# Performance work log

Measured on AMD Instinct MI355X. Metric: run time of the kernel, lower is better.

## Reference

```python
import jax, jax.numpy as jnp
import numpy as np

EPS = 1e-12

def _normalize(v):
    # matches F.normalize(..., eps): v / max(||v||, eps)
    return v / jnp.maximum(jnp.linalg.norm(v), EPS)

def sn_weight(W, u):
    """One power iteration (num_svs=1, num_itrs=1, eval mode: u not updated).
    W: [out, in] (1x1 conv flattened). u: [1, out].
    u, v are no-grad in torch; sv = v @ W.T @ u'.T carries grad w.r.t. W."""
    v = jax.lax.stop_gradient(_normalize(jax.lax.stop_gradient(u) @ W))          # [1, in]
    u2 = jax.lax.stop_gradient(_normalize(v @ W.T))                              # [1, out]
    sv = (v @ W.T @ u2.T)[0, 0]
    return W / sv

def maxpool2x2(x):
    B, C, H, W = x.shape
    return x.reshape(B, C, H // 2, 2, W // 2, 2).max(axis=(3, 5))

def conv1x1(W, x):
    # W: [out_c, in_c], x: [B, in_c, H, W]
    return jnp.einsum('oc,bchw->bohw', W, x)

def setup_inputs() -> dict:
    key = jax.random.key(0)
    ks = jax.random.split(key, 9)
    ch = 128
    B, H, W = 16, 64, 64
    x = jax.random.normal(ks[0], (B, ch, H, W), dtype=jnp.float32)
    # 1x1 conv weights flattened to [out, in], kaiming-ish scale
    def w(k, o, i):
        return jax.random.normal(k, (o, i), dtype=jnp.float32) * (1.0 / np.sqrt(i))
    w_theta = w(ks[1], ch // 8, ch)
    w_phi   = w(ks[2], ch // 8, ch)
    w_g     = w(ks[3], ch // 2, ch)
    w_o     = w(ks[4], ch, ch // 2)
    u_theta = jax.random.normal(ks[5], (1, ch // 8), dtype=jnp.float32)
    u_phi   = jax.random.normal(ks[6], (1, ch // 8), dtype=jnp.float32)
    u_g     = jax.random.normal(ks[7], (1, ch // 2), dtype=jnp.float32)
    u_o     = jax.random.normal(ks[8], (1, ch), dtype=jnp.float32)
    gamma = jnp.float32(0.7)  # param (init 0.0 in torch; nonzero for a meaningful test)
    return dict(x=x, w_theta=w_theta, w_phi=w_phi, w_g=w_g, w_o=w_o,
                u_theta=u_theta, u_phi=u_phi, u_g=u_g, u_o=u_o, gamma=gamma)

def reference(x, w_theta, w_phi, w_g, w_o, u_theta, u_phi, u_g, u_o, gamma):
    B, C, H, W = x.shape
    Wt = sn_weight(w_theta, u_theta)
    Wp = sn_weight(w_phi, u_phi)
    Wg = sn_weight(w_g, u_g)
    Wo = sn_weight(w_o, u_o)
    theta = conv1x1(Wt, x).reshape(B, C // 8, H * W)               # [B, C/8, HW]
    phi = maxpool2x2(conv1x1(Wp, x)).reshape(B, C // 8, H * W // 4)  # [B, C/8, HW/4]
    g = maxpool2x2(conv1x1(Wg, x)).reshape(B, C // 2, H * W // 4)    # [B, C/2, HW/4]
    beta = jax.nn.softmax(jnp.einsum('bcs,bct->bst', theta, phi), axis=-1)  # [B, HW, HW/4]
    o = jnp.einsum('bct,bst->bcs', g, beta).reshape(B, C // 2, H, W)
    return gamma * conv1x1(Wo, o) + x
```

## Files before the change

### kernel.cpp

```cpp
#include <hip/hip_runtime.h>
#include <hip/hip_bf16.h>


#define U_WN  0
#define U_WO  12288
#define U_TH  20480
#define U_PHI 1069056
#define U_G   1331200

typedef __attribute__((ext_vector_type(8))) short bf16x8;
typedef __attribute__((ext_vector_type(4))) short s16x4;
typedef __attribute__((ext_vector_type(4))) float f32x4;
typedef __attribute__((ext_vector_type(16))) float f32x16;

__device__ inline unsigned short f2b(float f) {
    union { float f; unsigned u; } v; v.f = f;
    unsigned r = v.u + 0x7FFFu + ((v.u >> 16) & 1u);
    return (unsigned short)(r >> 16);
}
__device__ inline float b2f(unsigned short u) {
    union { unsigned u; float f; } v; v.u = ((unsigned)u) << 16; return v.f;
}

__device__ inline unsigned cvtpk_bf16(float lo, float hi) {
    unsigned r;
    asm("s_nop 0\n\tv_cvt_pk_bf16_f32 %0, %1, %2" : "=v"(r) : "v"(lo), "v"(hi));
    return r;
}
__device__ inline void pl32swap(unsigned &a, unsigned &b) {
    asm("s_nop 1\n\tv_permlane32_swap_b32 %0, %1\n\ts_nop 1" : "+v"(a), "+v"(b));
}

__global__ __launch_bounds__(256) void sn4(
        const float* __restrict__ w0, const float* __restrict__ w1,
        const float* __restrict__ w2, const float* __restrict__ w3,
        const float* __restrict__ u0, const float* __restrict__ u1,
        const float* __restrict__ u2, const float* __restrict__ u3,
        unsigned short* __restrict__ wsu) {
    int wi = blockIdx.x;
    const float* W; const float* u; unsigned short* dst; int on, in_;
    if      (wi == 0) { W = w0; u = u0; dst = wsu;          on = 16;  in_ = 128; }
    else if (wi == 1) { W = w1; u = u1; dst = wsu + 2048;   on = 16;  in_ = 128; }
    else if (wi == 2) { W = w2; u = u2; dst = wsu + 4096;   on = 64;  in_ = 128; }
    else              { W = w3; u = u3; dst = wsu + 12288;  on = 128; in_ = 64;  }
    __shared__ float Wl[8320];
    __shared__ float ul[128];
    __shared__ float v[128];
    __shared__ float red[256];
    __shared__ float s_inv;
    int tid = threadIdx.x;
    int n = on * in_;
    int stride = in_ + 1;
    int shift = (in_ == 128) ? 7 : 6;
    int mask = in_ - 1;
    for (int i = tid; i < n; i += 256) {
        int o = i >> shift, j = i & mask;
        Wl[o * stride + j] = W[i];
    }
    if (tid < on) ul[tid] = u[tid];
    __syncthreads();
    float vi = 0.f;
    if (tid < in_) {
        for (int o = 0; o < on; ++o) vi += ul[o] * Wl[o * stride + tid];
    }
    red[tid] = (tid < in_) ? vi * vi : 0.f;
    __syncthreads();
    for (int st = 128; st > 0; st >>= 1) {
        if (tid < st) red[tid] += red[tid + st];
        __syncthreads();
    }
    float inv_nv = 1.0f / fmaxf(sqrtf(red[0]), 1e-12f);
    __syncthreads();
    if (tid < in_) v[tid] = vi * inv_nv;
    __syncthreads();
    float ui = 0.f;
    if (tid < on) {
        for (int i = 0; i < in_; ++i) ui += v[i] * Wl[tid * stride + i];
    }
    red[tid] = (tid < on) ? ui * ui : 0.f;
    __syncthreads();
    for (int st = 128; st > 0; st >>= 1) {
        if (tid < st) red[tid] += red[tid + st];
        __syncthreads();
    }
    if (tid == 0) {
        float nsq = red[0];
        float sv = nsq / fmaxf(sqrtf(nsq), 1e-12f);
        s_inv = 1.0f / sv;
    }
    __syncthreads();
    float inv = s_inv;
    for (int e = tid; e < n; e += 256) {
        int o = e >> shift, j = e & mask;
        dst[e] = f2b(Wl[o * stride + j] * inv);
    }
}

__global__ __launch_bounds__(512, 4) void convpool_mfma(
        const float* __restrict__ x, const unsigned short* __restrict__ wn,
        unsigned short* __restrict__ thetaT, unsigned short* __restrict__ phiT,
        unsigned short* __restrict__ gT) {
    __shared__ unsigned short xT[128 * 136];
    __shared__ unsigned short wnl[96 * 136];
    int tid = threadIdx.x;
    int bb = blockIdx.x >> 5, tile = blockIdx.x & 31;
    int px0 = tile << 7;
    for (int i = tid; i < 1536; i += 512) {
        int r = i >> 4, c8 = (i & 15) * 8;
        *(bf16x8*)&wnl[r * 136 + c8] = *(const bf16x8*)&wn[r * 128 + c8];
    }
    const float4* x4 = (const float4*)x;
    {
        int p4 = tid & 31, cg = (tid >> 5) * 4;
        for (int k = 0; k < 2; ++k) {
            int cb = k * 64 + cg;
            float4 v0 = x4[(bb * 128 + cb + 0) * 1024 + tile * 32 + p4];
            float4 v1 = x4[(bb * 128 + cb + 1) * 1024 + tile * 32 + p4];
            float4 v2 = x4[(bb * 128 + cb + 2) * 1024 + tile * 32 + p4];
            float4 v3 = x4[(bb * 128 + cb + 3) * 1024 + tile * 32 + p4];
            float a0[4] = {v0.x, v0.y, v0.z, v0.w};
            float a1[4] = {v1.x, v1.y, v1.z, v1.w};
            float a2[4] = {v2.x, v2.y, v2.z, v2.w};
            float a3[4] = {v3.x, v3.y, v3.z, v3.w};
#pragma unroll
            for (int j = 0; j < 4; ++j) {
                union { unsigned w[2]; s16x4 v; } pk;
                pk.w[0] = cvtpk_bf16(a0[j], a1[j]);
                pk.w[1] = cvtpk_bf16(a2[j], a3[j]);
                *(s16x4*)&xT[(p4 * 4 + j) * 136 + cb] = pk.v;
            }
        }
    }
    __syncthreads();
    int lane = tid & 63, wv = tid >> 6;
    int q = lane >> 4, l = lane & 15;
    int pxw = wv * 16;
    f32x4 acc[6];
    const f32x4 z4 = {0.f, 0.f, 0.f, 0.f};
#pragma unroll
    for (int nt = 0; nt < 6; ++nt) acc[nt] = z4;
#pragma unroll
    for (int kk = 0; kk < 4; ++kk) {
        bf16x8 a0 = *(const bf16x8*)&xT[(pxw + l) * 136 + kk * 32 + q * 8];
#pragma unroll
        for (int nt = 0; nt < 6; ++nt) {
            bf16x8 bw = *(const bf16x8*)&wnl[(nt * 16 + l) * 136 + kk * 32 + q * 8];
            acc[nt] = __builtin_amdgcn_mfma_f32_16x16x32_bf16(a0, bw, acc[nt], 0, 0, 0);
        }
    }
#pragma unroll
    for (int r = 0; r < 4; ++r) {
        int s = px0 + pxw + q * 4 + r;
        thetaT[(bb * 4096 + s) * 16 + l] = f2b(acc[0][r]);
    }
    __syncthreads();
    unsigned short* poolbuf = wnl;
#pragma unroll
    for (int nt = 1; nt < 6; ++nt) {
        int ch = nt * 16 + l - 16;
#pragma unroll
        for (int r = 0; r < 4; ++r) {
            poolbuf[ch * 132 + pxw + q * 4 + r] = f2b(acc[nt][r]);
        }
    }
    __syncthreads();
    for (int i = tid; i < 2560; i += 512) {
        int tcol = i & 31, ch = i >> 5;
        int base = ch * 132 + tcol * 2;
        float m0 = fmaxf(b2f(poolbuf[base]), b2f(poolbuf[base + 1]));
        float m1 = fmaxf(b2f(poolbuf[base + 64]), b2f(poolbuf[base + 65]));
        float m = fmaxf(m0, m1);
        int t = tile * 32 + tcol;
        if (ch < 16) phiT[(bb * 1024 + t) * 16 + ch] = f2b(m);
        else         gT[(bb * 64 + ch - 16) * 1024 + t] = f2b(m);
    }
}

__global__ __launch_bounds__(256, 4) void attn_out(
        const unsigned short* __restrict__ thetaT,
        const unsigned short* __restrict__ phiT,
        const unsigned short* __restrict__ gT,
        const unsigned short* __restrict__ wo,
        const float* __restrict__ x, const float* __restrict__ gam,
        float* __restrict__ out) {
    __shared__ unsigned short gl[2][2][4096];
    __shared__ float ldsD[2][2][32];
    float* ldsOf = (float*)&gl[0][0][0];
    int tid = threadIdx.x;
    int kblk = blockIdx.x;
    int vblk = (kblk & 7) * 128 + (kblk >> 3);
    int bb = vblk >> 6, st = vblk & 63;
    int s0 = st << 6;
    int lane = tid & 63, wv = tid >> 6;
    int sg = wv & 1, sp = wv >> 1;
    int sl = lane & 31, hi = lane >> 5;
    int srow = bb * 4096 + s0 + sg * 32 + sl;
    const unsigned short* phiB = phiT + bb * 16384;
    const unsigned short* gB   = gT + bb * 65536;
    int tbase = sp << 9;

    int sidx = tid & 127, shalf = tid >> 7;
    int src_c = sidx >> 1, spos = sidx & 1;
    const unsigned short* gsrc = gB + src_c * 1024 + shalf * 512 + spos * 32;
    unsigned short* glw = &gl[0][0][0];
    int wrow = src_c * 64;
    int wsw  = (src_c & 7) << 3;
    int wo_0 = (spos * 32 + 0)  ^ wsw, wo_1 = (spos * 32 + 8)  ^ wsw;
    int wo_2 = (spos * 32 + 16) ^ wsw, wo_3 = (spos * 32 + 24) ^ wsw;

    bf16x8 bth = *(const bf16x8*)&thetaT[srow * 16 + hi * 8];

    {
        bf16x8 r0 = *(const bf16x8*)&gsrc[0];
        bf16x8 r1 = *(const bf16x8*)&gsrc[8];
        bf16x8 r2 = *(const bf16x8*)&gsrc[16];
        bf16x8 r3 = *(const bf16x8*)&gsrc[24];
        unsigned short* d = &glw[shalf * 4096 + wrow];
        *(bf16x8*)&d[wo_0] = r0; *(bf16x8*)&d[wo_1] = r1;
        *(bf16x8*)&d[wo_2] = r2; *(bf16x8*)&d[wo_3] = r3;
    }

    f32x16 z16;
#pragma unroll
    for (int i = 0; i < 16; ++i) z16[i] = 0.f;
    f32x16 acc0 = z16, acc1 = z16;
    float lp4[4] = {0.f, 0.f, 0.f, 0.f};

    bf16x8 ph0 = *(const bf16x8*)&phiB[(tbase + sl) * 16 + hi * 8];
    bf16x8 ph1 = *(const bf16x8*)&phiB[(tbase + 32 + sl) * 16 + hi * 8];
    __syncthreads();

    int rsw = (sl & 7) << 3;
    for (int tc = 0; tc < 8; ++tc) {
        int buf = tc & 1;
        bf16x8 r0, r1, r2, r3;
        if (tc < 7) {
            const unsigned short* gs = gsrc + (tc + 1) * 64;
            r0 = *(const bf16x8*)&gs[0];
            r1 = *(const bf16x8*)&gs[8];
            r2 = *(const bf16x8*)&gs[16];
            r3 = *(const bf16x8*)&gs[24];
        }
        f32x16 sa = __builtin_amdgcn_mfma_f32_32x32x16_bf16(ph0, bth, z16, 0, 0, 0);
        unsigned u0[8], u1[8];
#pragma unroll
        for (int i = 0; i < 8; ++i) {
            float e0 = __expf(sa[2 * i]);
            float e1 = __expf(sa[2 * i + 1]);
            lp4[0] += e0; lp4[1] += e1;
            u0[i] = cvtpk_bf16(e0, e1);
        }
        __builtin_amdgcn_sched_barrier(0);
        f32x16 sb = __builtin_amdgcn_mfma_f32_32x32x16_bf16(ph1, bth, z16, 0, 0, 0);
        pl32swap(u0[0], u0[2]); pl32swap(u0[1], u0[3]);
        pl32swap(u0[4], u0[6]); pl32swap(u0[5], u0[7]);
        int t0n = tbase + (((tc + 1) & 7) << 6);
        ph0 = *(const bf16x8*)&phiB[(t0n + sl) * 16 + hi * 8];
        ph1 = *(const bf16x8*)&phiB[(t0n + 32 + sl) * 16 + hi * 8];
#pragma unroll
        for (int i = 0; i < 8; ++i) {
            float e2 = __expf(sb[2 * i]);
            float e3 = __expf(sb[2 * i + 1]);
            lp4[2] += e2; lp4[3] += e3;
            u1[i] = cvtpk_bf16(e2, e3);
        }
        pl32swap(u1[0], u1[2]); pl32swap(u1[1], u1[3]);
        pl32swap(u1[4], u1[6]); pl32swap(u1[5], u1[7]);
        const unsigned short* glr = &glw[(buf * 2 + sp) * 4096];
        __builtin_amdgcn_s_setprio(1);
        {
            int co = (0 * 16 + hi * 8) ^ rsw;
            bf16x8 gf0 = *(const bf16x8*)&glr[sl * 64 + co];
            bf16x8 gf1 = *(const bf16x8*)&glr[(32 + sl) * 64 + co];
            union { unsigned w[4]; bf16x8 v; } pf = {{u0[0], u0[1], u0[2], u0[3]}};
            acc0 = __builtin_amdgcn_mfma_f32_32x32x16_bf16(gf0, pf.v, acc0, 0, 0, 0);
            acc1 = __builtin_amdgcn_mfma_f32_32x32x16_bf16(gf1, pf.v, acc1, 0, 0, 0);
        }
        {
            int co = (1 * 16 + hi * 8) ^ rsw;
            bf16x8 gf0 = *(const bf16x8*)&glr[sl * 64 + co];
            bf16x8 gf1 = *(const bf16x8*)&glr[(32 + sl) * 64 + co];
            union { unsigned w[4]; bf16x8 v; } pf = {{u0[4], u0[5], u0[6], u0[7]}};
            acc0 = __builtin_amdgcn_mfma_f32_32x32x16_bf16(gf0, pf.v, acc0, 0, 0, 0);
            acc1 = __builtin_amdgcn_mfma_f32_32x32x16_bf16(gf1, pf.v, acc1, 0, 0, 0);
        }
        {
            int co = (2 * 16 + hi * 8) ^ rsw;
            bf16x8 gf0 = *(const bf16x8*)&glr[sl * 64 + co];
            bf16x8 gf1 = *(const bf16x8*)&glr[(32 + sl) * 64 + co];
            union { unsigned w[4]; bf16x8 v; } pf = {{u1[0], u1[1], u1[2], u1[3]}};
            acc0 = __builtin_amdgcn_mfma_f32_32x32x16_bf16(gf0, pf.v, acc0, 0, 0, 0);
            acc1 = __builtin_amdgcn_mfma_f32_32x32x16_bf16(gf1, pf.v, acc1, 0, 0, 0);
        }
        {
            int co = (3 * 16 + hi * 8) ^ rsw;
            bf16x8 gf0 = *(const bf16x8*)&glr[sl * 64 + co];
            bf16x8 gf1 = *(const bf16x8*)&glr[(32 + sl) * 64 + co];
            union { unsigned w[4]; bf16x8 v; } pf = {{u1[4], u1[5], u1[6], u1[7]}};
            acc0 = __builtin_amdgcn_mfma_f32_32x32x16_bf16(gf0, pf.v, acc0, 0, 0, 0);
            acc1 = __builtin_amdgcn_mfma_f32_32x32x16_bf16(gf1, pf.v, acc1, 0, 0, 0);
        }
        __builtin_amdgcn_s_setprio(0);
        if (tc < 7) {
            unsigned short* d = &glw[((buf ^ 1) * 2 + shalf) * 4096 + wrow];
            *(bf16x8*)&d[wo_0] = r0; *(bf16x8*)&d[wo_1] = r1;
            *(bf16x8*)&d[wo_2] = r2; *(bf16x8*)&d[wo_3] = r3;
            __syncthreads();
        }
    }
    __syncthreads();

    float tot = (lp4[0] + lp4[1]) + (lp4[2] + lp4[3]);
    tot += __shfl_xor(tot, 32);

#pragma unroll
    for (int i = 0; i < 16; ++i) {
        int c = (i & 3) + 8 * (i >> 2) + 4 * hi;
        ldsOf[(sg * 2 + sp) * 2048 + c * 32 + sl] = acc0[i];
        ldsOf[(sg * 2 + sp) * 2048 + (32 + c) * 32 + sl] = acc1[i];
    }
    if (hi == 0) ldsD[sg][sp][sl] = tot;
    bf16x8 aw[2][4];
#pragma unroll
    for (int mt = 0; mt < 2; ++mt)
#pragma unroll
        for (int ch = 0; ch < 4; ++ch)
            aw[mt][ch] = *(const bf16x8*)&wo[(sp * 64 + mt * 32 + sl) * 64 + ch * 16 + hi * 8];
    __syncthreads();
    int osp = sp ^ 1;
    tot += ldsD[sg][osp][sl];
    float inv = 1.0f / tot;
#pragma unroll
    for (int i = 0; i < 16; ++i) {
        int c = (i & 3) + 8 * (i >> 2) + 4 * hi;
        acc0[i] += ldsOf[(sg * 2 + osp) * 2048 + c * 32 + sl];
        acc1[i] += ldsOf[(sg * 2 + osp) * 2048 + (32 + c) * 32 + sl];
    }
    unsigned o0[8], o1[8];
#pragma unroll
    for (int i = 0; i < 8; ++i) {
        o0[i] = cvtpk_bf16(acc0[2 * i] * inv, acc0[2 * i + 1] * inv);
        o1[i] = cvtpk_bf16(acc1[2 * i] * inv, acc1[2 * i + 1] * inv);
    }
    pl32swap(o0[0], o0[2]); pl32swap(o0[1], o0[3]);
    pl32swap(o0[4], o0[6]); pl32swap(o0[5], o0[7]);
    pl32swap(o1[0], o1[2]); pl32swap(o1[1], o1[3]);
    pl32swap(o1[4], o1[6]); pl32swap(o1[5], o1[7]);
    bf16x8 bfr[4];
    {
        union { unsigned w[4]; bf16x8 v; } t;
        t.w[0] = o0[0]; t.w[1] = o0[1]; t.w[2] = o0[2]; t.w[3] = o0[3]; bfr[0] = t.v;
        t.w[0] = o0[4]; t.w[1] = o0[5]; t.w[2] = o0[6]; t.w[3] = o0[7]; bfr[1] = t.v;
        t.w[0] = o1[0]; t.w[1] = o1[1]; t.w[2] = o1[2]; t.w[3] = o1[3]; bfr[2] = t.v;
        t.w[0] = o1[4]; t.w[1] = o1[5]; t.w[2] = o1[6]; t.w[3] = o1[7]; bfr[3] = t.v;
    }
    f32x16 d0 = z16, d1 = z16;
#pragma unroll
    for (int ch = 0; ch < 4; ++ch) {
        d0 = __builtin_amdgcn_mfma_f32_32x32x16_bf16(aw[0][ch], bfr[ch], d0, 0, 0, 0);
        d1 = __builtin_amdgcn_mfma_f32_32x32x16_bf16(aw[1][ch], bfr[ch], d1, 0, 0, 0);
    }
    float gm = gam[0];
    int scol = s0 + sg * 32 + sl;
#pragma unroll
    for (int i = 0; i < 16; ++i) {
        int r = (i & 3) + 8 * (i >> 2) + 4 * hi;
        int a0 = (bb * 128 + sp * 64 + r) * 4096 + scol;
        int a1 = (bb * 128 + sp * 64 + 32 + r) * 4096 + scol;
        out[a0] = gm * d0[i] + x[a0];
        out[a1] = gm * d1[i] + x[a1];
    }
}

extern "C" void kernel_launch(void* const* d_in, const int* in_sizes, int n_in,
                              void* d_out, int out_size, void* d_ws, size_t ws_size,
                              hipStream_t stream) {
    const float* x  = (const float*)d_in[0];
    const float* wt = (const float*)d_in[1];
    const float* wp = (const float*)d_in[2];
    const float* wg = (const float*)d_in[3];
    const float* wo = (const float*)d_in[4];
    const float* ut = (const float*)d_in[5];
    const float* up = (const float*)d_in[6];
    const float* ug = (const float*)d_in[7];
    const float* uo = (const float*)d_in[8];
    const float* gm = (const float*)d_in[9];
    unsigned short* wsu = (unsigned short*)d_ws;
    float* out = (float*)d_out;

    sn4<<<4, 256, 0, stream>>>(wt, wp, wg, wo, ut, up, ug, uo, wsu);
    convpool_mfma<<<512, 512, 0, stream>>>(x, wsu + U_WN,
                                           wsu + U_TH, wsu + U_PHI, wsu + U_G);
    attn_out<<<1024, 256, 0, stream>>>(wsu + U_TH, wsu + U_PHI, wsu + U_G,
                                       wsu + U_WO, x, gm, out);
}
```

Measured before the change: 134.0 us.

## Stream g tiles to LDS with direct global_load_lds and interleave second exp block

Replaces the register-staged global-to-LDS copy of the g tile (load into VGPRs, then swizzled ds_write) with direct global_load_lds 16-byte transfers, with the swizzle folded into the source address. The second softmax exp block and the phi prefetch move between the first and second halves of the PV MFMAs so exp work overlaps with matrix work. This is meant to cut VGPR pressure and LDS write instructions and to improve overlap. It relies on the barrier ordering the async LDS loads, and no explicit vmcnt wait is visible before the sync.

```diff
diff --git a/kernel.cpp b/kernel.cpp
--- a/kernel.cpp
+++ b/kernel.cpp
@@ -29,6 +29,11 @@
 }
 __device__ inline void pl32swap(unsigned &a, unsigned &b) {
     asm("s_nop 1\n\tv_permlane32_swap_b32 %0, %1\n\ts_nop 1" : "+v"(a), "+v"(b));
+}
+__device__ inline void gload_lds16(const unsigned short* g, unsigned short* l) {
+    __builtin_amdgcn_global_load_lds(
+        (const __attribute__((address_space(1))) unsigned int*)g,
+        (__attribute__((address_space(3))) unsigned int*)l, 16, 0, 0);
 }
 
 __global__ __launch_bounds__(256) void sn4(
@@ -199,26 +204,15 @@
     const unsigned short* gB   = gT + bb * 65536;
     int tbase = sp << 9;
 
-    int sidx = tid & 127, shalf = tid >> 7;
-    int src_c = sidx >> 1, spos = sidx & 1;
-    const unsigned short* gsrc = gB + src_c * 1024 + shalf * 512 + spos * 32;
-    unsigned short* glw = &gl[0][0][0];
-    int wrow = src_c * 64;
-    int wsw  = (src_c & 7) << 3;
-    int wo_0 = (spos * 32 + 0)  ^ wsw, wo_1 = (spos * 32 + 8)  ^ wsw;
-    int wo_2 = (spos * 32 + 16) ^ wsw, wo_3 = (spos * 32 + 24) ^ wsw;
+    int h = wv >> 1;
+    int rb = (wv & 1) * 32;
+    int cl = lane >> 3, js = lane & 7;
+    const unsigned short* gsl = gB + (rb + cl) * 1024 + h * 512 + ((js ^ cl) * 8);
+#pragma unroll
+    for (int k = 0; k < 4; ++k)
+        gload_lds16(gsl + k * 8192, &gl[0][h][(rb + k * 8) * 64]);
 
     bf16x8 bth = *(const bf16x8*)&thetaT[srow * 16 + hi * 8];
-
-    {
-        bf16x8 r0 = *(const bf16x8*)&gsrc[0];
-        bf16x8 r1 = *(const bf16x8*)&gsrc[8];
-        bf16x8 r2 = *(const bf16x8*)&gsrc[16];
-        bf16x8 r3 = *(const bf16x8*)&gsrc[24];
-        unsigned short* d = &glw[shalf * 4096 + wrow];
-        *(bf16x8*)&d[wo_0] = r0; *(bf16x8*)&d[wo_1] = r1;
-        *(bf16x8*)&d[wo_2] = r2; *(bf16x8*)&d[wo_3] = r3;
-    }
 
     f32x16 z16;
 #pragma unroll
@@ -233,13 +227,11 @@
     int rsw = (sl & 7) << 3;
     for (int tc = 0; tc < 8; ++tc) {
         int buf = tc & 1;
-        bf16x8 r0, r1, r2, r3;
         if (tc < 7) {
-            const unsigned short* gs = gsrc + (tc + 1) * 64;
-            r0 = *(const bf16x8*)&gs[0];
-            r1 = *(const bf16x8*)&gs[8];
-            r2 = *(const bf16x8*)&gs[16];
-            r3 = *(const bf16x8*)&gs[24];
+#pragma unroll
+            for (int k = 0; k < 4; ++k)
+                gload_lds16(gsl + k * 8192 + (tc + 1) * 64,
+                            &gl[buf ^ 1][h][(rb + k * 8) * 64]);
         }
         f32x16 sa = __builtin_amdgcn_mfma_f32_32x32x16_bf16(ph0, bth, z16, 0, 0, 0);
         unsigned u0[8], u1[8];
@@ -254,19 +246,7 @@
         f32x16 sb = __builtin_amdgcn_mfma_f32_32x32x16_bf16(ph1, bth, z16, 0, 0, 0);
         pl32swap(u0[0], u0[2]); pl32swap(u0[1], u0[3]);
         pl32swap(u0[4], u0[6]); pl32swap(u0[5], u0[7]);
-        int t0n = tbase + (((tc + 1) & 7) << 6);
-        ph0 = *(const bf16x8*)&phiB[(t0n + sl) * 16 + hi * 8];
-        ph1 = *(const bf16x8*)&phiB[(t0n + 32 + sl) * 16 + hi * 8];
-#pragma unroll
-        for (int i = 0; i < 8; ++i) {
-            float e2 = __expf(sb[2 * i]);
-            float e3 = __expf(sb[2 * i + 1]);
-            lp4[2] += e2; lp4[3] += e3;
-            u1[i] = cvtpk_bf16(e2, e3);
-        }
-        pl32swap(u1[0], u1[2]); pl32swap(u1[1], u1[3]);
-        pl32swap(u1[4], u1[6]); pl32swap(u1[5], u1[7]);
-        const unsigned short* glr = &glw[(buf * 2 + sp) * 4096];
+        const unsigned short* glr = &gl[buf][sp][0];
         __builtin_amdgcn_s_setprio(1);
         {
             int co = (0 * 16 + hi * 8) ^ rsw;
@@ -284,6 +264,20 @@
             acc0 = __builtin_amdgcn_mfma_f32_32x32x16_bf16(gf0, pf.v, acc0, 0, 0, 0);
             acc1 = __builtin_amdgcn_mfma_f32_32x32x16_bf16(gf1, pf.v, acc1, 0, 0, 0);
         }
+        __builtin_amdgcn_s_setprio(0);
+        int t0n = tbase + (((tc + 1) & 7) << 6);
+        ph0 = *(const bf16x8*)&phiB[(t0n + sl) * 16 + hi * 8];
+        ph1 = *(const bf16x8*)&phiB[(t0n + 32 + sl) * 16 + hi * 8];
+#pragma unroll
+        for (int i = 0; i < 8; ++i) {
+            float e2 = __expf(sb[2 * i]);
+            float e3 = __expf(sb[2 * i + 1]);
+            lp4[2] += e2; lp4[3] += e3;
+            u1[i] = cvtpk_bf16(e2, e3);
+        }
+        pl32swap(u1[0], u1[2]); pl32swap(u1[1], u1[3]);
+        pl32swap(u1[4], u1[6]); pl32swap(u1[5], u1[7]);
+        __builtin_amdgcn_s_setprio(1);
         {
             int co = (2 * 16 + hi * 8) ^ rsw;
             bf16x8 gf0 = *(const bf16x8*)&glr[sl * 64 + co];
@@ -301,12 +295,7 @@
             acc1 = __builtin_amdgcn_mfma_f32_32x32x16_bf16(gf1, pf.v, acc1, 0, 0, 0);
         }
         __builtin_amdgcn_s_setprio(0);
-        if (tc < 7) {
-            unsigned short* d = &glw[((buf ^ 1) * 2 + shalf) * 4096 + wrow];
-            *(bf16x8*)&d[wo_0] = r0; *(bf16x8*)&d[wo_1] = r1;
-            *(bf16x8*)&d[wo_2] = r2; *(bf16x8*)&d[wo_3] = r3;
-            __syncthreads();
-        }
+        if (tc < 7) __syncthreads();
     }
     __syncthreads();
 
```

After: 131.7 us. About the same (-1.7%).
